# Optimization experiments

Measured on AMD Instinct MI355X. Metric: run time of the kernel, lower is better.

## Reference

```python
import jax, jax.numpy as jnp
import numpy as np

TINY = 1e-6  # TINY_NUMBER in the source repo
H, W, S = 256, 512, 64
N = H * W

def _unit(x, axis=-1):
    return x / jnp.maximum(jnp.linalg.norm(x, axis=axis, keepdims=True), 1e-4)

def setup_inputs() -> dict:
    key = jax.random.key(0)
    ks = jax.random.split(key, 9)
    normal = _unit(jax.random.normal(ks[0], (H, W, 3), jnp.float32))
    albedo = jax.random.uniform(ks[1], (H, W, 3), jnp.float32)
    roughness = jax.random.uniform(ks[2], (H, W, 1), jnp.float32)
    points = jax.random.normal(ks[3], (H, W, 3), jnp.float32)
    cam_position = jax.random.normal(ks[4], (3,), jnp.float32)
    light_dir_diff = _unit(jax.random.normal(ks[5], (N, S, 3), jnp.float32))
    diffuse_lighting = jax.random.uniform(ks[6], (N, S, 3), jnp.float32)
    h_dir_specular = _unit(jax.random.normal(ks[7], (N, S, 3), jnp.float32))
    specular_lighting = jax.random.uniform(ks[8], (N, S, 3), jnp.float32)
    return {"normal": normal, "albedo": albedo, "roughness": roughness,
            "points": points, "cam_position": cam_position,
            "light_dir_diff": light_dir_diff, "diffuse_lighting": diffuse_lighting,
            "h_dir_specular": h_dir_specular, "specular_lighting": specular_lighting}

def reference(normal, albedo, roughness, points, cam_position,
              light_dir_diff, diffuse_lighting, h_dir_specular, specular_lighting):
    env_h, env_w, _ = normal.shape
    n = normal.reshape(-1, 3)        # [N,3]
    a = albedo.reshape(-1, 3)        # [N,3]
    r = roughness.reshape(-1, 1)     # [N,1]
    p = points.reshape(-1, 3)        # [N,3]
    # view = F.normalize(cam - p, eps=1e-4): x / clamp(||x||, min=eps)
    d = cam_position[None, :] - p
    view = d / jnp.maximum(jnp.linalg.norm(d, axis=-1, keepdims=True), 1e-4)  # [N,3]

    def cdot(x, y):  # clamped dot over last axis, keepdim -> [...,1]
        return jnp.clip(jnp.sum(x * y, axis=-1, keepdims=True), 0.0, 1.0)

    # ---- diffuse: sum_s L * (albedo/pi) * ndl * 2*pi / S ----
    ndl_d = cdot(n[:, None, :], light_dir_diff)                      # [N,S,1]
    diffuse = jnp.sum(diffuse_lighting * (a[:, None, :] / np.pi) * ndl_d
                      * (2.0 * np.pi), axis=1) / S                   # [N,3]

    # ---- specular: GGX-style split-sum with importance-sampled half vectors ----
    v = view[:, None, :]                                             # [N,1,3]
    h = h_dir_specular                                               # [N,S,3]
    vdh = cdot(h, v)                                                 # [N,S,1]
    l_spec = 2.0 * vdh * h - v                                       # [N,S,3]
    ndl = cdot(n[:, None, :], l_spec)                                # [N,S,1]
    ndh = cdot(n[:, None, :], h)                                     # [N,S,1]
    ndv = cdot(n, view)[:, None, :]                                  # [N,1,1]
    f = 0.04 + 0.96 * jnp.exp2((-5.55472 * vdh - 6.98316) * vdh)     # Fresnel approx
    k = (r[:, None, :] + 1.0) ** 2 / 8.0                             # [N,1,1]
    g1_ndv = ndv / jnp.maximum(ndv * (1.0 - k) + k, TINY)
    g1_ndl = ndl / jnp.maximum(ndl * (1.0 - k) + k, TINY)
    brdf = f * (g1_ndl * g1_ndv) / jnp.maximum(4.0 * ndl * ndv, TINY)
    specular = jnp.sum(specular_lighting * brdf * ndl * 4.0 * vdh
                       / jnp.maximum(ndh, TINY), axis=1) / S         # [N,3]

    return (diffuse + specular).reshape(env_h, env_w, 3)
```

## Files before the change

kernel.cpp:

```cpp
#include <hip/hip_runtime.h>

#define TINY 1e-6f

constexpr int N_PIX = 256 * 512;

struct f3 { float x, y, z; };

__device__ __forceinline__ float clamp01(float x) {
    return fminf(fmaxf(x, 0.0f), 1.0f);
}

__device__ __forceinline__ float frcp(float x) {
    return __builtin_amdgcn_rcpf(x);
}

__global__ void __launch_bounds__(256, 2)
shade_kernel(const float* __restrict__ normal,
             const float* __restrict__ albedo,
             const float* __restrict__ roughness,
             const float* __restrict__ points,
             const float* __restrict__ cam,
             const float* __restrict__ ldir,
             const float* __restrict__ dlight,
             const float* __restrict__ hdir,
             const float* __restrict__ slight,
             float* __restrict__ out)
{
    const int tid = blockIdx.x * 256 + threadIdx.x;
    const int pix = tid >> 4;
    const int sub = tid & 15;

    const size_t pbase = (size_t)pix * 192;
    const int    loff  = sub * 3;

    f3 Lv[4], Dv[4], Hv[4], Sv[4];
#pragma unroll
    for (int k = 0; k < 4; ++k) {
        const size_t o = pbase + (size_t)(k * 48 + loff);
        Lv[k] = *(const f3*)(ldir   + o);
        Dv[k] = *(const f3*)(dlight + o);
        Hv[k] = *(const f3*)(hdir   + o);
        Sv[k] = *(const f3*)(slight + o);
    }

    const float nx = normal[pix * 3 + 0];
    const float ny = normal[pix * 3 + 1];
    const float nz = normal[pix * 3 + 2];
    const float r  = roughness[pix];
    const float px = points[pix * 3 + 0];
    const float py = points[pix * 3 + 1];
    const float pz = points[pix * 3 + 2];
    const float cx = cam[0], cy = cam[1], cz = cam[2];

    const float dx = cx - px, dy = cy - py, dz = cz - pz;
    const float len = sqrtf(dx * dx + dy * dy + dz * dz);
    const float inv = frcp(fmaxf(len, 1e-4f));
    const float vx = dx * inv, vy = dy * inv, vz = dz * inv;

    const float ndv = clamp01(nx * vx + ny * vy + nz * vz);
    const float k1  = (r + 1.0f) * (r + 1.0f) * 0.125f;
    const float omk = 1.0f - k1;
    const float g1v = ndv * frcp(fmaxf(ndv * omk + k1, TINY));

    float dacc0 = 0.f, dacc1 = 0.f, dacc2 = 0.f;
    float sacc0 = 0.f, sacc1 = 0.f, sacc2 = 0.f;

#pragma unroll
    for (int j = 0; j < 4; ++j) {
        const float lx = Lv[j].x, ly = Lv[j].y, lz = Lv[j].z;
        const float d0 = Dv[j].x, d1 = Dv[j].y, d2 = Dv[j].z;
        const float hx = Hv[j].x, hy = Hv[j].y, hz = Hv[j].z;
        const float s0 = Sv[j].x, s1 = Sv[j].y, s2 = Sv[j].z;

        const float ndl_d = clamp01(nx * lx + ny * ly + nz * lz);
        dacc0 += d0 * ndl_d;
        dacc1 += d1 * ndl_d;
        dacc2 += d2 * ndl_d;

        const float vdh = clamp01(hx * vx + hy * vy + hz * vz);
        const float tv  = 2.0f * vdh;
        const float lsx = tv * hx - vx;
        const float lsy = tv * hy - vy;
        const float lsz = tv * hz - vz;
        const float ndl = clamp01(nx * lsx + ny * lsy + nz * lsz);
        const float ndh = clamp01(nx * hx + ny * hy + nz * hz);
        const float f   = 0.04f + 0.96f * exp2f((-5.55472f * vdh - 6.98316f) * vdh);
        const float g1l = ndl * frcp(fmaxf(ndl * omk + k1, TINY));
        const float brdf = f * g1l * g1v * frcp(fmaxf(4.0f * ndl * ndv, TINY));
        const float wgt  = brdf * ndl * 4.0f * vdh * frcp(fmaxf(ndh, TINY));
        sacc0 += s0 * wgt;
        sacc1 += s1 * wgt;
        sacc2 += s2 * wgt;
    }

#pragma unroll
    for (int off = 1; off < 16; off <<= 1) {
        dacc0 += __shfl_xor(dacc0, off);
        dacc1 += __shfl_xor(dacc1, off);
        dacc2 += __shfl_xor(dacc2, off);
        sacc0 += __shfl_xor(sacc0, off);
        sacc1 += __shfl_xor(sacc1, off);
        sacc2 += __shfl_xor(sacc2, off);
    }

    if (sub == 0) {
        const float ax = albedo[pix * 3 + 0];
        const float ay = albedo[pix * 3 + 1];
        const float az = albedo[pix * 3 + 2];
        const float inv_s = 1.0f / 64.0f;
        out[pix * 3 + 0] = (dacc0 * ax * 2.0f + sacc0) * inv_s;
        out[pix * 3 + 1] = (dacc1 * ay * 2.0f + sacc1) * inv_s;
        out[pix * 3 + 2] = (dacc2 * az * 2.0f + sacc2) * inv_s;
    }
}

extern "C" void kernel_launch(void* const* d_in, const int* in_sizes, int n_in,
                              void* d_out, int out_size, void* d_ws, size_t ws_size,
                              hipStream_t stream) {
    const float* normal    = (const float*)d_in[0];
    const float* albedo    = (const float*)d_in[1];
    const float* roughness = (const float*)d_in[2];
    const float* points    = (const float*)d_in[3];
    const float* cam       = (const float*)d_in[4];
    const float* ldir      = (const float*)d_in[5];
    const float* dlight    = (const float*)d_in[6];
    const float* hdir      = (const float*)d_in[7];
    const float* slight    = (const float*)d_in[8];
    float* out = (float*)d_out;

    const int blocks = N_PIX / 16;
    shade_kernel<<<blocks, 256, 0, stream>>>(normal, albedo, roughness, points,
                                             cam, ldir, dlight, hdir, slight, out);
}
```

Baseline: 349.2 us.

## Stage per-pixel sample arrays through LDS with coalesced float4 loads

Replaces the strided 12-byte per-thread global loads of the four sample arrays with fully coalesced float4 loads by the whole block into padded shared memory. Threads then read their pixel's samples from LDS. The launch-bounds occupancy hint goes from 2 to 3 blocks. The change targets uncoalesced global access, at the cost of about 50 KB of LDS per block, a block barrier, and possible LDS bank conflicts.

```diff
diff --git a/kernel.cpp b/kernel.cpp
--- a/kernel.cpp
+++ b/kernel.cpp
@@ -3,8 +3,8 @@
 #define TINY 1e-6f
 
 constexpr int N_PIX = 256 * 512;
-
-struct f3 { float x, y, z; };
+constexpr int TILE  = 16;
+constexpr int PPAD  = 196;
 
 __device__ __forceinline__ float clamp01(float x) {
     return fminf(fmaxf(x, 0.0f), 1.0f);
@@ -14,7 +14,7 @@
     return __builtin_amdgcn_rcpf(x);
 }
 
-__global__ void __launch_bounds__(256, 2)
+__global__ void __launch_bounds__(256, 3)
 shade_kernel(const float* __restrict__ normal,
              const float* __restrict__ albedo,
              const float* __restrict__ roughness,
@@ -26,22 +26,39 @@
              const float* __restrict__ slight,
              float* __restrict__ out)
 {
-    const int tid = blockIdx.x * 256 + threadIdx.x;
-    const int pix = tid >> 4;
-    const int sub = tid & 15;
+    __shared__ float lds[4][TILE * PPAD];
 
-    const size_t pbase = (size_t)pix * 192;
-    const int    loff  = sub * 3;
+    const int t      = threadIdx.x;
+    const int stage0 = blockIdx.x * TILE;
 
-    f3 Lv[4], Dv[4], Hv[4], Sv[4];
+    const float* garr[4] = { ldir, dlight, hdir, slight };
+    float4 v[4][3];
 #pragma unroll
-    for (int k = 0; k < 4; ++k) {
-        const size_t o = pbase + (size_t)(k * 48 + loff);
-        Lv[k] = *(const f3*)(ldir   + o);
-        Dv[k] = *(const f3*)(dlight + o);
-        Hv[k] = *(const f3*)(hdir   + o);
-        Sv[k] = *(const f3*)(slight + o);
+    for (int a = 0; a < 4; ++a) {
+        const float4* g = (const float4*)(garr[a] + (size_t)stage0 * 192);
+#pragma unroll
+        for (int c = 0; c < 3; ++c)
+            v[a][c] = g[c * 256 + t];
     }
+    __builtin_amdgcn_sched_barrier(0);
+
+#pragma unroll
+    for (int a = 0; a < 4; ++a) {
+#pragma unroll
+        for (int c = 0; c < 3; ++c) {
+            const int f   = c * 256 + t;
+            const int p   = f / 48;
+            const int rem = f - p * 48;
+            *(float4*)&lds[a][p * PPAD + rem * 4] = v[a][c];
+        }
+    }
+
+    const int w    = t >> 6;
+    const int lane = t & 63;
+    const int grp  = lane >> 4;
+    const int sub  = lane & 15;
+    const int pin  = w * 4 + grp;
+    const int pix  = stage0 + pin;
 
     const float nx = normal[pix * 3 + 0];
     const float ny = normal[pix * 3 + 1];
@@ -62,15 +79,23 @@
     const float omk = 1.0f - k1;
     const float g1v = ndv * frcp(fmaxf(ndv * omk + k1, TINY));
 
+    __syncthreads();
+
+    const float* Lb = &lds[0][pin * PPAD];
+    const float* Db = &lds[1][pin * PPAD];
+    const float* Hb = &lds[2][pin * PPAD];
+    const float* Sb = &lds[3][pin * PPAD];
+
     float dacc0 = 0.f, dacc1 = 0.f, dacc2 = 0.f;
     float sacc0 = 0.f, sacc1 = 0.f, sacc2 = 0.f;
 
 #pragma unroll
     for (int j = 0; j < 4; ++j) {
-        const float lx = Lv[j].x, ly = Lv[j].y, lz = Lv[j].z;
-        const float d0 = Dv[j].x, d1 = Dv[j].y, d2 = Dv[j].z;
-        const float hx = Hv[j].x, hy = Hv[j].y, hz = Hv[j].z;
-        const float s0 = Sv[j].x, s1 = Sv[j].y, s2 = Sv[j].z;
+        const int o = j * 48 + sub * 3;
+        const float lx = Lb[o + 0], ly = Lb[o + 1], lz = Lb[o + 2];
+        const float d0 = Db[o + 0], d1 = Db[o + 1], d2 = Db[o + 2];
+        const float hx = Hb[o + 0], hy = Hb[o + 1], hz = Hb[o + 2];
+        const float s0 = Sb[o + 0], s1 = Sb[o + 1], s2 = Sb[o + 2];
 
         const float ndl_d = clamp01(nx * lx + ny * ly + nz * lz);
         dacc0 += d0 * ndl_d;
@@ -128,7 +153,7 @@
     const float* slight    = (const float*)d_in[8];
     float* out = (float*)d_out;
 
-    const int blocks = N_PIX / 16;
+    const int blocks = N_PIX / TILE;
     shade_kernel<<<blocks, 256, 0, stream>>>(normal, albedo, roughness, points,
                                              cam, ldir, dlight, hdir, slight, out);
 }
```

Result: slower. 413.1 us (+18.3%).
